# Kernel tuning notes

Hardware: AMD Instinct MI355X
Metric: run time of the kernel (lower is better)

## Reference

```python
import jax, jax.numpy as jnp
import numpy as np

B, T, H, I, O, R = 64, 1024, 1024, 8, 8, 4
NOISE_STD, ALPHA = 0.05, 0.2


def setup_inputs() -> dict:
    key = jax.random.key(0)
    ks = jax.random.split(key, 6)
    return {
        "x": jax.random.normal(ks[0], (B, T, I), jnp.float32),
        "noise": jax.random.normal(ks[1], (B, T, H), jnp.float32),
        "wi": jax.random.normal(ks[2], (I, H), jnp.float32),
        "si": jnp.ones((I,), jnp.float32),
        "m": jax.random.normal(ks[3], (H, R), jnp.float32),
        "n": jax.random.normal(ks[4], (H, R), jnp.float32),
        "b": jnp.zeros((H,), jnp.float32),
        "wo": jax.random.normal(ks[5], (H, O), jnp.float32) / H,
        "so": jnp.ones((O,), jnp.float32),
        "h0": jnp.zeros((H,), jnp.float32),
    }


def reference(x, noise, wi, si, m, n, b, wo, so, h0):
    hidden = h0.shape[0]
    batch = x.shape[0]
    wi_full = wi * si[:, None]          # (I, H): (wi.T * si).T
    wo_full = wo * so                   # (H, O)
    h_init = jnp.broadcast_to(h0, (batch, hidden))
    r_init = jnp.tanh(h_init)           # non_linearity(initial_states)
    # precompute input drive for all steps: (B,T,H) -> scan over time-major
    u = jnp.einsum('bti,ih->tbh', x, wi_full)
    noise_t = jnp.transpose(noise, (1, 0, 2))  # (T,B,H)

    def step(carry, inp):
        h, r = carry
        u_i, nz_i = inp
        rec = (r @ n) @ m.T / hidden                    # low-rank recurrence
        h = h + NOISE_STD * nz_i + ALPHA * (-h + rec + u_i)
        r = jnp.tanh(h + b)
        out = h @ wo_full                               # identity output nonlin
        return (h, r), out

    _, outs = jax.lax.scan(step, (h_init, r_init), (u, noise_t))
    return jnp.transpose(outs, (1, 0, 2))  # (B,T,O)
```

## Files before the change

kernel.cpp:

```cpp
#include <hip/hip_runtime.h>

#define BB 64
#define TT 1024
#define HH 1024
#define II 8
#define OO 8
#define RRK 4
#define NOISE_STD 0.05f
#define ALPHA 0.2f

template<int CTRL, int RM>
__device__ __forceinline__ float dpp_add(float acc, float src) {
    int s = __builtin_amdgcn_update_dpp(0, __float_as_int(src), CTRL, RM, 0xF, true);
    return acc + __int_as_float(s);
}

__device__ __forceinline__ float wave_sum(float x) {
    x = dpp_add<0xB1, 0xF>(x, x);
    x = dpp_add<0x4E, 0xF>(x, x);
    x = dpp_add<0x141, 0xF>(x, x);
    x = dpp_add<0x140, 0xF>(x, x);
    x = dpp_add<0x142, 0xA>(x, x);
    x = dpp_add<0x143, 0xC>(x, x);
    return x;
}

__device__ __forceinline__ float tanh_from_2x(float two_x) {
    float e = __expf(two_x);
    float r = __builtin_amdgcn_rcpf(e + 1.0f);
    return fmaf(-2.0f, r, 1.0f);
}

__device__ __forceinline__ void block_sync_lds() {
    asm volatile("s_waitcnt lgkmcnt(0)\n\ts_barrier" ::: "memory");
}

__global__ __launch_bounds__(256)
void prew_kernel(const float* __restrict__ noise, const float* __restrict__ wo,
                 const float* __restrict__ so, float* __restrict__ W) {
    __shared__ __align__(16) float red[4][4][8];

    const int tid  = threadIdx.x;
    const int wave = tid >> 6;
    const int lane = tid & 63;
    const int e0   = tid << 2;

    float woa[4][OO];
    {
        float so8[OO];
        #pragma unroll
        for (int o = 0; o < OO; ++o) so8[o] = so[o] * NOISE_STD;
        #pragma unroll
        for (int e = 0; e < 4; ++e) {
            const float4 a4 = *(const float4*)(wo + (e0 + e) * OO);
            const float4 b4 = *(const float4*)(wo + (e0 + e) * OO + 4);
            woa[e][0] = a4.x * so8[0]; woa[e][1] = a4.y * so8[1];
            woa[e][2] = a4.z * so8[2]; woa[e][3] = a4.w * so8[3];
            woa[e][4] = b4.x * so8[4]; woa[e][5] = b4.y * so8[5];
            woa[e][6] = b4.z * so8[6]; woa[e][7] = b4.w * so8[7];
        }
    }

    const int row0 = blockIdx.x * 32;
    for (int g = 0; g < 8; ++g) {
        #pragma unroll
        for (int j = 0; j < 4; ++j) {
            const int row = row0 + g * 4 + j;
            const float4 nz = *(const float4*)(noise + (size_t)row * HH + e0);
            float op[OO];
            #pragma unroll
            for (int o = 0; o < OO; ++o)
                op[o] = fmaf(nz.x, woa[0][o], fmaf(nz.y, woa[1][o],
                        fmaf(nz.z, woa[2][o], nz.w * woa[3][o])));
            #pragma unroll
            for (int o = 0; o < OO; ++o) op[o] = wave_sum(op[o]);
            if (lane == 63) {
                *(float4*)&red[j][wave][0] = make_float4(op[0], op[1], op[2], op[3]);
                *(float4*)&red[j][wave][4] = make_float4(op[4], op[5], op[6], op[7]);
            }
        }
        block_sync_lds();
        if (tid < 32) {
            const int j = tid >> 3, o = tid & 7;
            const int row = row0 + g * 4 + j;
            W[row * OO + o] = (red[j][0][o] + red[j][1][o]) +
                              (red[j][2][o] + red[j][3][o]);
        }
        block_sync_lds();
    }
}

__global__ __launch_bounds__(256, 1)
void rnn_seq_kernel(const float* __restrict__ x, const float* __restrict__ noise,
                    const float* __restrict__ wi, const float* __restrict__ si,
                    const float* __restrict__ mM, const float* __restrict__ nM,
                    const float* __restrict__ bv, const float* __restrict__ wo,
                    const float* __restrict__ so, const float* __restrict__ h0,
                    const float* __restrict__ W, float* __restrict__ out) {
    __shared__ __align__(16) float lds_x[TT * II];
    __shared__ __align__(16) float lds_W[TT * OO];
    __shared__ __align__(16) float lds_out[TT * OO];
    __shared__ __align__(16) float red[4][4][4];
    __shared__ __align__(16) float redc[4][104];
    __shared__ float ambx[104];

    const int tid  = threadIdx.x;
    const int b    = blockIdx.x;
    const int wave = tid >> 6;
    const int lane = tid & 63;
    const int e0   = tid << 2;
    const int oc   = tid & 7;

    {
        const float4* sx = (const float4*)(x + (size_t)b * (TT * II));
        const float4* sw = (const float4*)(W + (size_t)b * (TT * OO));
        float4* dx = (float4*)lds_x;
        float4* dw = (float4*)lds_W;
        #pragma unroll
        for (int k = 0; k < 8; ++k) {
            dx[k * 256 + tid] = sx[k * 256 + tid];
            dw[k * 256 + tid] = sw[k * 256 + tid];
        }
    }

    float wia[II][4];
    #pragma unroll
    for (int i = 0; i < II; ++i) {
        const float s  = ALPHA * si[i];
        const float4 w = *(const float4*)(wi + i * HH + e0);
        wia[i][0] = w.x * s; wia[i][1] = w.y * s; wia[i][2] = w.z * s; wia[i][3] = w.w * s;
    }
    float ma[4][RRK], nr[4][RRK];
    #pragma unroll
    for (int e = 0; e < 4; ++e) {
        const float4 m4 = *(const float4*)(mM + (e0 + e) * RRK);
        const float4 n4 = *(const float4*)(nM + (e0 + e) * RRK);
        const float cs = ALPHA / (float)HH;
        ma[e][0] = m4.x * cs; ma[e][1] = m4.y * cs; ma[e][2] = m4.z * cs; ma[e][3] = m4.w * cs;
        nr[e][0] = n4.x; nr[e][1] = n4.y; nr[e][2] = n4.z; nr[e][3] = n4.w;
    }
    float woa[4][OO];
    {
        float so8[OO];
        #pragma unroll
        for (int o = 0; o < OO; ++o) so8[o] = so[o];
        #pragma unroll
        for (int e = 0; e < 4; ++e) {
            const float4 a4 = *(const float4*)(wo + (e0 + e) * OO);
            const float4 b4 = *(const float4*)(wo + (e0 + e) * OO + 4);
            woa[e][0] = a4.x * so8[0]; woa[e][1] = a4.y * so8[1];
            woa[e][2] = a4.z * so8[2]; woa[e][3] = a4.w * so8[3];
            woa[e][4] = b4.x * so8[4]; woa[e][5] = b4.y * so8[5];
            woa[e][6] = b4.z * so8[6]; woa[e][7] = b4.w * so8[7];
        }
    }
    float tb2[4], h[4], r[4];
    {
        const float4 b4 = *(const float4*)(bv + e0);
        tb2[0] = 2.f * b4.x; tb2[1] = 2.f * b4.y; tb2[2] = 2.f * b4.z; tb2[3] = 2.f * b4.w;
        const float4 h4 = *(const float4*)(h0 + e0);
        h[0] = h4.x; h[1] = h4.y; h[2] = h4.z; h[3] = h4.w;
        #pragma unroll
        for (int e = 0; e < 4; ++e) r[e] = tanh_from_2x(2.f * h[e]);
    }

    #pragma unroll
    for (int kg = 0; kg < 26; ++kg) {
        float p[4];
        #pragma unroll
        for (int u = 0; u < 4; ++u) {
            const int k = kg * 4 + u;
            float s;
            if (k < 32) {
                const int q = k >> 3, o = k & 7;
                s = fmaf(ma[0][q], woa[0][o], fmaf(ma[1][q], woa[1][o],
                    fmaf(ma[2][q], woa[2][o], ma[3][q] * woa[3][o])));
            } else if (k < 96) {
                const int i = (k - 32) >> 3, o = k & 7;
                s = fmaf(wia[i][0], woa[0][o], fmaf(wia[i][1], woa[1][o],
                    fmaf(wia[i][2], woa[2][o], wia[i][3] * woa[3][o])));
            } else {
                const int o = k - 96;
                s = fmaf(h[0], woa[0][o], fmaf(h[1], woa[1][o],
                    fmaf(h[2], woa[2][o], h[3] * woa[3][o])));
            }
            p[u] = wave_sum(s);
        }
        if (lane == 63)
            *(float4*)&redc[wave][kg * 4] = make_float4(p[0], p[1], p[2], p[3]);
    }
    block_sync_lds();
    if (tid < 104)
        ambx[tid] = (redc[0][tid] + redc[1][tid]) + (redc[2][tid] + redc[3][tid]);
    __syncthreads();

    float Amr[RRK], Bxr[II], y;
    #pragma unroll
    for (int q = 0; q < RRK; ++q) Amr[q] = ambx[q * 8 + oc];
    #pragma unroll
    for (int i = 0; i < II; ++i) Bxr[i] = ambx[32 + i * 8 + oc];
    y = ambx[96 + oc];

    const float* nzp = noise + (size_t)b * (TT * HH) + e0;
    float4 nzb[4];
    #pragma unroll
    for (int j = 0; j < 4; ++j) nzb[j] = *(const float4*)(nzp + (size_t)j * HH);

    float4 xqc0 = *(const float4*)&lds_x[0];
    float4 xqc1 = *(const float4*)&lds_x[4];
    float  wqc  = lds_W[oc];

    for (int t0 = 0; t0 < TT; t0 += 4) {
        #pragma unroll
        for (int j = 0; j < 4; ++j) {
            const int t = t0 + j;

            const int tn = (t + 1 < TT) ? t + 1 : TT - 1;
            const float4 xqn0 = *(const float4*)&lds_x[tn * II];
            const float4 xqn1 = *(const float4*)&lds_x[tn * II + 4];
            const float  wqn  = lds_W[tn * OO + oc];

            float vp[RRK];
            #pragma unroll
            for (int q = 0; q < RRK; ++q)
                vp[q] = fmaf(r[0], nr[0][q], fmaf(r[1], nr[1][q],
                        fmaf(r[2], nr[2][q], r[3] * nr[3][q])));
            #pragma unroll
            for (int q = 0; q < RRK; ++q) vp[q] = wave_sum(vp[q]);
            if (lane == 63)
                *(float4*)&red[j][wave][0] = make_float4(vp[0], vp[1], vp[2], vp[3]);

            float ybase = fmaf(xqc0.x, Bxr[0], wqc);
            ybase = fmaf(xqc0.y, Bxr[1], ybase);
            ybase = fmaf(xqc0.z, Bxr[2], ybase);
            ybase = fmaf(xqc0.w, Bxr[3], ybase);
            ybase = fmaf(xqc1.x, Bxr[4], ybase);
            ybase = fmaf(xqc1.y, Bxr[5], ybase);
            ybase = fmaf(xqc1.z, Bxr[6], ybase);
            ybase = fmaf(xqc1.w, Bxr[7], ybase);

            float au[4];
            #pragma unroll
            for (int e = 0; e < 4; ++e) {
                float a = xqc0.x * wia[0][e];
                a = fmaf(xqc0.y, wia[1][e], a);
                a = fmaf(xqc0.z, wia[2][e], a);
                a = fmaf(xqc0.w, wia[3][e], a);
                a = fmaf(xqc1.x, wia[4][e], a);
                a = fmaf(xqc1.y, wia[5][e], a);
                a = fmaf(xqc1.z, wia[6][e], a);
                au[e] = fmaf(xqc1.w, wia[7][e], a);
            }

            block_sync_lds();

            const float4 s0 = *(const float4*)&red[j][0][0];
            const float4 s1 = *(const float4*)&red[j][1][0];
            const float4 s2 = *(const float4*)&red[j][2][0];
            const float4 s3 = *(const float4*)&red[j][3][0];
            const float v0 = (s0.x + s1.x) + (s2.x + s3.x);
            const float v1 = (s0.y + s1.y) + (s2.y + s3.y);
            const float v2 = (s0.z + s1.z) + (s2.z + s3.z);
            const float v3 = (s0.w + s1.w) + (s2.w + s3.w);

            const float nzv[4] = {nzb[j].x, nzb[j].y, nzb[j].z, nzb[j].w};
            #pragma unroll
            for (int e = 0; e < 4; ++e) {
                float acc = au[e];
                acc = fmaf(v0, ma[e][0], acc);
                acc = fmaf(v1, ma[e][1], acc);
                acc = fmaf(v2, ma[e][2], acc);
                acc = fmaf(v3, ma[e][3], acc);
                h[e] = fmaf(NOISE_STD, nzv[e], fmaf(1.0f - ALPHA, h[e], acc));
            }

            {
                float t4 = fmaf(v0, Amr[0], ybase);
                t4 = fmaf(v1, Amr[1], t4);
                t4 = fmaf(v2, Amr[2], t4);
                t4 = fmaf(v3, Amr[3], t4);
                y = fmaf(1.0f - ALPHA, y, t4);
                if (tid < OO) lds_out[t * OO + tid] = y;
            }

            {
                int tf = t + 4; if (tf >= TT) tf = 0;
                nzb[j] = *(const float4*)(nzp + (size_t)tf * HH);
            }

            #pragma unroll
            for (int e = 0; e < 4; ++e)
                r[e] = tanh_from_2x(fmaf(2.0f, h[e], tb2[e]));

            xqc0 = xqn0; xqc1 = xqn1; wqc = wqn;
        }
    }

    __syncthreads();
    {
        float4* dst = (float4*)(out + (size_t)b * (TT * OO));
        const float4* srcv = (const float4*)lds_out;
        #pragma unroll
        for (int k = 0; k < 8; ++k)
            dst[k * 256 + tid] = srcv[k * 256 + tid];
    }
}

extern "C" void kernel_launch(void* const* d_in, const int* in_sizes, int n_in,
                              void* d_out, int out_size, void* d_ws, size_t ws_size,
                              hipStream_t stream) {
    const float* x     = (const float*)d_in[0];
    const float* noise = (const float*)d_in[1];
    const float* wi    = (const float*)d_in[2];
    const float* si    = (const float*)d_in[3];
    const float* mM    = (const float*)d_in[4];
    const float* nM    = (const float*)d_in[5];
    const float* bv    = (const float*)d_in[6];
    const float* wo    = (const float*)d_in[7];
    const float* so    = (const float*)d_in[8];
    const float* h0    = (const float*)d_in[9];
    float* out = (float*)d_out;
    float* W   = (float*)d_ws;

    prew_kernel<<<dim3(2048), dim3(256), 0, stream>>>(noise, wo, so, W);
    rnn_seq_kernel<<<dim3(BB), dim3(256), 0, stream>>>(
        x, noise, wi, si, mM, nM, bv, wo, so, h0, W, out);
}
```

Measured before the change: 848.5 us.

## Pack two batch sequences per 512-thread block and store outputs directly to global

Each workgroup now runs two independent batch rows as two 256-thread teams, with per-team LDS buffers. The grid halves to 32 blocks of 512 threads. The LDS output staging buffer and the final copy loop are removed; each step's output is written straight to global memory. The cost is that the per-step block barrier now spans 8 waves and couples the two teams, and fewer blocks run on the device.

```diff
diff --git a/kernel.cpp b/kernel.cpp
--- a/kernel.cpp
+++ b/kernel.cpp
@@ -90,36 +90,38 @@
     }
 }
 
-__global__ __launch_bounds__(256, 1)
+__global__ __launch_bounds__(512, 2)
 void rnn_seq_kernel(const float* __restrict__ x, const float* __restrict__ noise,
                     const float* __restrict__ wi, const float* __restrict__ si,
                     const float* __restrict__ mM, const float* __restrict__ nM,
                     const float* __restrict__ bv, const float* __restrict__ wo,
                     const float* __restrict__ so, const float* __restrict__ h0,
                     const float* __restrict__ W, float* __restrict__ out) {
-    __shared__ __align__(16) float lds_x[TT * II];
-    __shared__ __align__(16) float lds_W[TT * OO];
-    __shared__ __align__(16) float lds_out[TT * OO];
-    __shared__ __align__(16) float red[4][4][4];
-    __shared__ __align__(16) float redc[4][104];
-    __shared__ float ambx[104];
+    __shared__ __align__(16) float lds_x[2][TT * II];
+    __shared__ __align__(16) float lds_W[2][TT * OO];
+    __shared__ __align__(16) float red[2][4][4][4];
+    __shared__ __align__(16) float redc[2][4][104];
+    __shared__ float ambx[2][104];
 
     const int tid  = threadIdx.x;
-    const int b    = blockIdx.x;
     const int wave = tid >> 6;
+    const int team = wave >> 2;
+    const int tw   = wave & 3;
+    const int ttid = tid & 255;
     const int lane = tid & 63;
-    const int e0   = tid << 2;
-    const int oc   = tid & 7;
+    const int e0   = ttid << 2;
+    const int oc   = ttid & 7;
+    const int b    = blockIdx.x * 2 + team;
 
     {
         const float4* sx = (const float4*)(x + (size_t)b * (TT * II));
         const float4* sw = (const float4*)(W + (size_t)b * (TT * OO));
-        float4* dx = (float4*)lds_x;
-        float4* dw = (float4*)lds_W;
+        float4* dx = (float4*)lds_x[team];
+        float4* dw = (float4*)lds_W[team];
         #pragma unroll
         for (int k = 0; k < 8; ++k) {
-            dx[k * 256 + tid] = sx[k * 256 + tid];
-            dw[k * 256 + tid] = sw[k * 256 + tid];
+            dx[k * 256 + ttid] = sx[k * 256 + ttid];
+            dw[k * 256 + ttid] = sw[k * 256 + ttid];
         }
     }
 
@@ -187,28 +189,31 @@
             p[u] = wave_sum(s);
         }
         if (lane == 63)
-            *(float4*)&redc[wave][kg * 4] = make_float4(p[0], p[1], p[2], p[3]);
+            *(float4*)&redc[team][tw][kg * 4] = make_float4(p[0], p[1], p[2], p[3]);
     }
     block_sync_lds();
-    if (tid < 104)
-        ambx[tid] = (redc[0][tid] + redc[1][tid]) + (redc[2][tid] + redc[3][tid]);
+    if (ttid < 104)
+        ambx[team][ttid] = (redc[team][0][ttid] + redc[team][1][ttid]) +
+                           (redc[team][2][ttid] + redc[team][3][ttid]);
     __syncthreads();
 
     float Amr[RRK], Bxr[II], y;
     #pragma unroll
-    for (int q = 0; q < RRK; ++q) Amr[q] = ambx[q * 8 + oc];
-    #pragma unroll
-    for (int i = 0; i < II; ++i) Bxr[i] = ambx[32 + i * 8 + oc];
-    y = ambx[96 + oc];
+    for (int q = 0; q < RRK; ++q) Amr[q] = ambx[team][q * 8 + oc];
+    #pragma unroll
+    for (int i = 0; i < II; ++i) Bxr[i] = ambx[team][32 + i * 8 + oc];
+    y = ambx[team][96 + oc];
 
     const float* nzp = noise + (size_t)b * (TT * HH) + e0;
     float4 nzb[4];
     #pragma unroll
     for (int j = 0; j < 4; ++j) nzb[j] = *(const float4*)(nzp + (size_t)j * HH);
 
-    float4 xqc0 = *(const float4*)&lds_x[0];
-    float4 xqc1 = *(const float4*)&lds_x[4];
-    float  wqc  = lds_W[oc];
+    float4 xqc0 = *(const float4*)&lds_x[team][0];
+    float4 xqc1 = *(const float4*)&lds_x[team][4];
+    float  wqc  = lds_W[team][oc];
+
+    float* outb = out + (size_t)b * (TT * OO);
 
     for (int t0 = 0; t0 < TT; t0 += 4) {
         #pragma unroll
@@ -216,9 +221,9 @@
             const int t = t0 + j;
 
             const int tn = (t + 1 < TT) ? t + 1 : TT - 1;
-            const float4 xqn0 = *(const float4*)&lds_x[tn * II];
-            const float4 xqn1 = *(const float4*)&lds_x[tn * II + 4];
-            const float  wqn  = lds_W[tn * OO + oc];
+            const float4 xqn0 = *(const float4*)&lds_x[team][tn * II];
+            const float4 xqn1 = *(const float4*)&lds_x[team][tn * II + 4];
+            const float  wqn  = lds_W[team][tn * OO + oc];
 
             float vp[RRK];
             #pragma unroll
@@ -228,7 +233,7 @@
             #pragma unroll
             for (int q = 0; q < RRK; ++q) vp[q] = wave_sum(vp[q]);
             if (lane == 63)
-                *(float4*)&red[j][wave][0] = make_float4(vp[0], vp[1], vp[2], vp[3]);
+                *(float4*)&red[team][j][tw][0] = make_float4(vp[0], vp[1], vp[2], vp[3]);
 
             float ybase = fmaf(xqc0.x, Bxr[0], wqc);
             ybase = fmaf(xqc0.y, Bxr[1], ybase);
@@ -254,10 +259,10 @@
 
             block_sync_lds();
 
-            const float4 s0 = *(const float4*)&red[j][0][0];
-            const float4 s1 = *(const float4*)&red[j][1][0];
-            const float4 s2 = *(const float4*)&red[j][2][0];
-            const float4 s3 = *(const float4*)&red[j][3][0];
+            const float4 s0 = *(const float4*)&red[team][j][0][0];
+            const float4 s1 = *(const float4*)&red[team][j][1][0];
+            const float4 s2 = *(const float4*)&red[team][j][2][0];
+            const float4 s3 = *(const float4*)&red[team][j][3][0];
             const float v0 = (s0.x + s1.x) + (s2.x + s3.x);
             const float v1 = (s0.y + s1.y) + (s2.y + s3.y);
             const float v2 = (s0.z + s1.z) + (s2.z + s3.z);
@@ -280,7 +285,7 @@
                 t4 = fmaf(v2, Amr[2], t4);
                 t4 = fmaf(v3, Amr[3], t4);
                 y = fmaf(1.0f - ALPHA, y, t4);
-                if (tid < OO) lds_out[t * OO + tid] = y;
+                if (ttid < OO) outb[t * OO + ttid] = y;
             }
 
             {
@@ -294,15 +299,6 @@
 
             xqc0 = xqn0; xqc1 = xqn1; wqc = wqn;
         }
-    }
-
-    __syncthreads();
-    {
-        float4* dst = (float4*)(out + (size_t)b * (TT * OO));
-        const float4* srcv = (const float4*)lds_out;
-        #pragma unroll
-        for (int k = 0; k < 8; ++k)
-            dst[k * 256 + tid] = srcv[k * 256 + tid];
     }
 }
 
@@ -323,6 +319,6 @@
     float* W   = (float*)d_ws;
 
     prew_kernel<<<dim3(2048), dim3(256), 0, stream>>>(noise, wo, so, W);
-    rnn_seq_kernel<<<dim3(BB), dim3(256), 0, stream>>>(
+    rnn_seq_kernel<<<dim3(BB / 2), dim3(512), 0, stream>>>(
         x, noise, wi, si, mM, nM, bv, wo, so, h0, W, out);
 }
```

After: 1.006 ms. +18.5%, slower.
